# Kernel optimization log

Hardware: AMD Instinct MI355X
Metric: run time of the kernel (lower is better)

Reference implementation:

```python
import jax, jax.numpy as jnp
import numpy as np

C_NUM, D_NUM = 64, 128
N_NODES = C_NUM * D_NUM + C_NUM + D_NUM  # 8384
HEADS, OUT = 4, 256


def gat_conv(h, src, dst, W, al, ar, b):
    """DGL-style GATConv (eval mode, attn_drop off). h:[N,F], W:[F,H*O], al/ar:[H,O], b:[H*O]."""
    N = h.shape[0]
    H, O = al.shape
    feat = (h @ W).reshape(N, H, O)
    el = jnp.sum(feat * al, axis=-1)                      # [N,H]
    er = jnp.sum(feat * ar, axis=-1)
    e = jax.nn.leaky_relu(el[src] + er[dst], 0.2)         # [E,H]
    m = jax.ops.segment_max(e, dst, num_segments=N)
    m = jnp.where(jnp.isfinite(m), m, 0.0)
    p = jnp.exp(e - m[dst])
    s = jax.ops.segment_sum(p, dst, num_segments=N)
    a = p / jnp.maximum(s[dst], 1e-9)                     # edge softmax per dst, per head
    out = jax.ops.segment_sum(a[:, :, None] * feat[src], dst, num_segments=N)  # [N,H,O]
    return out + b.reshape(1, H, O)


def cagat_layer(edges, dfeat, cvec, gw, al, ar, gb,
                wq_w, wq_b, wk_w, wk_b, wv_w, wv_b, ip_w, ip_b, op_w, op_b):
    ch = cvec.shape[1]
    pad = jnp.repeat(cvec, D_NUM, axis=0)                       # [c*d, ch]
    pad3 = jnp.broadcast_to(cvec.mean(axis=0), (D_NUM, ch))      # [d, ch]
    cfin = jnp.concatenate([pad, cvec, pad3], axis=0)            # [N, ch]
    inf = jnp.concatenate([dfeat, cfin], axis=1)                 # [N, F+ch]
    # 4 relation-specific GATConvs, stacked (HeteroGraphConv aggregate='stack')
    rst = jnp.stack([gat_conv(inf, edges[t, 0], edges[t, 1], gw[t], al[t], ar[t], gb[t])
                     for t in range(4)], axis=1)                 # [N,4,H,O]
    N = inf.shape[0]
    rst = rst.reshape(N, 4 * HEADS, OUT)
    E = OUT
    Q = (cfin @ wq_w + wq_b)[:, None, :]                         # [N,1,E]
    K = rst @ wk_w + wk_b                                        # [N,16,E]
    V = rst @ wv_w + wv_b
    # nn.MultiheadAttention(E, 1): in-proj then single-head SDPA then out-proj
    q = Q @ ip_w[:E].T + ip_b[:E]
    k = K @ ip_w[E:2 * E].T + ip_b[E:2 * E]
    v = V @ ip_w[2 * E:].T + ip_b[2 * E:]
    att = jax.nn.softmax(jnp.einsum('nqe,nke->nqk', q, k) / jnp.sqrt(jnp.float32(E)), axis=-1)
    o = jnp.einsum('nqk,nke->nqe', att, v) @ op_w.T + op_b
    return o.reshape(N, E)


def setup_inputs() -> dict:
    key = jax.random.key(0)
    ks = iter(jax.random.split(key, 64))
    rn = lambda shape: jax.random.normal(next(ks), shape, jnp.float32) * 0.05
    inp = {}
    inp['x'] = rn((D_NUM, 256))
    inp['cf'] = rn((C_NUM, 512))
    inp['cf_net_w'] = rn((512, 128)); inp['cf_net_b'] = rn((128,))
    inp['ht_w'] = rn((512, 256)); inp['ht_b'] = rn((256,))
    for l in ('1', '2'):
        inp['gw' + l] = rn((4, 384, HEADS * OUT))
        inp['al' + l] = rn((4, HEADS, OUT))
        inp['ar' + l] = rn((4, HEADS, OUT))
        inp['gb' + l] = rn((4, HEADS * OUT))
        inp['wq' + l + '_w'] = rn((128, 256)); inp['wq' + l + '_b'] = rn((256,))
        inp['wk' + l + '_w'] = rn((256, 256)); inp['wk' + l + '_b'] = rn((256,))
        inp['wv' + l + '_w'] = rn((256, 256)); inp['wv' + l + '_b'] = rn((256,))
        inp['ip' + l + '_w'] = rn((768, 256)); inp['ip' + l + '_b'] = rn((768,))
        inp['op' + l + '_w'] = rn((256, 256)); inp['op' + l + '_b'] = rn((256,))
    inp['edges'] = jax.random.randint(next(ks), (4, 2, 50000), 0, N_NODES, dtype=jnp.int32)
    return inp


def reference(x, cf, cf_net_w, cf_net_b, ht_w, ht_b,
              gw1, al1, ar1, gb1, wq1_w, wq1_b, wk1_w, wk1_b, wv1_w, wv1_b, ip1_w, ip1_b, op1_w, op1_b,
              gw2, al2, ar2, gb2, wq2_w, wq2_b, wk2_w, wk2_b, wv2_w, wv2_b, ip2_w, ip2_b, op2_w, op2_b,
              edges):
    cf_vec = cf @ cf_net_w + cf_net_b                           # [c, cell_hidden]
    d_pad = jnp.tile(x, (C_NUM, 1))                             # [c*d, in]
    d_uc = cf @ ht_w + ht_b                                     # [c, in]
    d_feat = jnp.concatenate([d_pad, d_uc, x], axis=0)          # [N, in]
    h = cagat_layer(edges, d_feat, cf_vec, gw1, al1, ar1, gb1,
                    wq1_w, wq1_b, wk1_w, wk1_b, wv1_w, wv1_b, ip1_w, ip1_b, op1_w, op1_b)
    h = cagat_layer(edges, h, cf_vec, gw2, al2, ar2, gb2,
                    wq2_w, wq2_b, wk2_w, wk2_b, wv2_w, wv2_b, ip2_w, ip2_b, op2_w, op2_b)
    return h
```

## Files before the change

kernel.cpp:

```cpp
#include <hip/hip_runtime.h>
#include <hip/hip_bf16.h>

typedef __hip_bfloat16 bf16;
typedef __attribute__((ext_vector_type(8))) short short8;
typedef __attribute__((ext_vector_type(4))) short short4v;
typedef __attribute__((ext_vector_type(4))) float f32x4;

#define KN 8384
#define KNPAD 8448
#define KE 50000
#define NBIG 4480

__device__ __forceinline__ float toF(float v){ return v; }
__device__ __forceinline__ float toF(bf16 v){ return __bfloat162float(v); }
__device__ __forceinline__ float b2f(short u){ return __uint_as_float(((unsigned int)(unsigned short)u) << 16); }
__device__ __forceinline__ void stor(float* p, float v){ *p = v; }
__device__ __forceinline__ void stor(bf16* p, float v){ *p = __float2bfloat16(v); }

__device__ __forceinline__ void glds16(const bf16* g, bf16* l){
  __builtin_amdgcn_global_load_lds(
      (const __attribute__((address_space(1))) unsigned int*)(g),
      (__attribute__((address_space(3))) unsigned int*)(l), 16, 0, 0);
}

template<typename TC>
__global__ __launch_bounds__(256)
void gemm_mfma_bt(const bf16* __restrict__ A, const bf16* __restrict__ BT,
                  const float* __restrict__ bias, TC* __restrict__ C,
                  int M, int N, int K, int ldc, int nbx)
{
  __shared__ bf16 As[3][128 * 32];
  __shared__ bf16 Bs[3][128 * 32];
  const int nwg = gridDim.x;
  const int q = nwg >> 3, r = nwg & 7;
  const int xcd = blockIdx.x & 7, idx = blockIdx.x >> 3;
  const int sw = (xcd < r) ? xcd * (q + 1) + idx : r * (q + 1) + (xcd - r) * q + idx;
  const int bn = (sw % nbx) * 128, bm = (sw / nbx) * 128;
  const int tid = threadIdx.x;
  const int w = tid >> 6, l = tid & 63;
  const int wr = (w >> 1) * 64, wc = (w & 1) * 64;
  const int lr = l & 15;
  int rS[2], lqS[2];
  #pragma unroll
  for (int i = 0; i < 2; i++){
    rS[i] = w * 32 + i * 16 + (l >> 2);
    lqS[i] = (l & 3) ^ ((rS[i] >> 1) & 3);
  }
  const bf16* gA0 = A  + (size_t)(bm + rS[0]) * K + lqS[0] * 8;
  const bf16* gA1 = A  + (size_t)(bm + rS[1]) * K + lqS[1] * 8;
  const bf16* gB0 = BT + (size_t)(bn + rS[0]) * K + lqS[0] * 8;
  const bf16* gB1 = BT + (size_t)(bn + rS[1]) * K + lqS[1] * 8;
  const int nt = K >> 5;
  auto issue = [&](int t){
    int b = t - (t / 3) * 3;
    int k0 = t << 5;
    glds16(gA0 + k0, &As[b][w * 1024]);
    glds16(gA1 + k0, &As[b][w * 1024 + 512]);
    glds16(gB0 + k0, &Bs[b][w * 1024]);
    glds16(gB1 + k0, &Bs[b][w * 1024 + 512]);
  };
  f32x4 acc[4][4] = {};
  issue(0);
  issue(1);
  for (int t = 0; t < nt; t++){
    if (t < nt - 1) asm volatile("s_waitcnt vmcnt(4)\ns_barrier" ::: "memory");
    else            asm volatile("s_waitcnt vmcnt(0)\ns_barrier" ::: "memory");
    if (t + 2 < nt) issue(t + 2);
    int b = t - (t / 3) * 3;
    short8 a[4], bb[4];
    #pragma unroll
    for (int i = 0; i < 4; i++){
      int R = wr + i * 16 + lr;
      int pq = (l >> 4) ^ ((R >> 1) & 3);
      a[i] = *(short8*)&As[b][R * 32 + pq * 8];
    }
    #pragma unroll
    for (int j = 0; j < 4; j++){
      int R = wc + j * 16 + lr;
      int pq = (l >> 4) ^ ((R >> 1) & 3);
      bb[j] = *(short8*)&Bs[b][R * 32 + pq * 8];
    }
    #pragma unroll
    for (int i = 0; i < 4; i++)
      #pragma unroll
      for (int j = 0; j < 4; j++)
        acc[i][j] = __builtin_amdgcn_mfma_f32_16x16x32_bf16(a[i], bb[j], acc[i][j], 0, 0, 0);
  }
  const int orow = (l >> 4) * 4, ocol = l & 15;
  #pragma unroll
  for (int i = 0; i < 4; i++){
    #pragma unroll
    for (int j = 0; j < 4; j++){
      int gcol = bn + wc + j * 16 + ocol;
      float bv = bias ? bias[gcol] : 0.f;
      #pragma unroll
      for (int rg = 0; rg < 4; rg++){
        int grow = bm + wr + i * 16 + orow + rg;
        if (grow < M) stor(&C[(size_t)grow * ldc + gcol], acc[i][j][rg] + bv);
      }
    }
  }
}

struct LPtrs {
  const float *gw[2], *al[2], *ar[2];
  const float *wqw[2], *wqb[2], *wkw[2], *wvw[2], *wvb[2];
  const float *ipw[2], *ipb[2], *opw[2], *opb[2];
  bf16* bigBT[2];
  float *ipwQT[2], *wkwT[2], *opwT[2], *wvwT[2];
  float *Wq[2], *B2[2], *M1[2], *bq[2];
  bf16* WvT[2];
  float *bv[2], *biasc[2];
  int* cnt;
};

#define PT0 1536
#define PT1 4608
#define PT2 4864
#define PT3 5248
#define PT4 5392
#define PT5 5524
__global__ __launch_bounds__(256)
void k_prep_all(LPtrs P){
  const int lay = blockIdx.z;
  const int b = blockIdx.x, tid = threadIdx.x;
  bf16* bigBT = P.bigBT[lay];
  if (b < PT0){
    __shared__ float t[32][33];
    int rel = b / 384, rem = b % 384;
    int n0 = (rem % 32) * 32, k0 = (rem / 32) * 32;
    const float* B = P.gw[lay] + (size_t)rel * 384 * 1024;
    bf16* BT = bigBT + (size_t)rel * 1024 * 384;
    int tx = tid & 31, ty = tid >> 5;
    for (int i = ty; i < 32; i += 8)
      t[i][tx] = B[(size_t)(k0 + i) * 1024 + n0 + tx];
    __syncthreads();
    for (int i = ty; i < 32; i += 8)
      BT[(size_t)(n0 + i) * 384 + k0 + tx] = __float2bfloat16(t[tx][i]);
  } else if (b < PT1){
    int bb = b - PT0;
    int kblk = bb % 96, r = bb / 96;
    int k = kblk * 4 + (tid >> 6), lane = tid & 63;
    int rr = r & 15, t = rr >> 2, h = rr & 3;
    const float* wsrc = ((r < 16) ? P.al[lay] : P.ar[lay]) + t * 1024 + h * 256;
    const float* gp = P.gw[lay] + (size_t)t * 384 * 1024 + (size_t)k * 1024 + h * 256;
    float v = 0.f;
    #pragma unroll
    for (int i = 0; i < 4; i++){
      int o = lane + i * 64;
      v += gp[o] * wsrc[o];
    }
    #pragma unroll
    for (int off = 32; off; off >>= 1) v += __shfl_down(v, off);
    if (lane == 0) bigBT[(size_t)(4352 + r) * 384 + k] = __float2bfloat16(v);
  } else if (b < PT2){
    __shared__ float t[32][33];
    int bb = b - PT1;
    int mat = bb >> 6, rem = bb & 63;
    int c0 = (rem & 7) * 32, r0 = (rem >> 3) * 32;
    const float* S; float* D;
    switch (mat){
      case 0: S = P.ipw[lay]; D = P.ipwQT[lay]; break;
      case 1: S = P.wkw[lay]; D = P.wkwT[lay]; break;
      case 2: S = P.opw[lay]; D = P.opwT[lay]; break;
      default: S = P.wvw[lay]; D = P.wvwT[lay]; break;
    }
    int tx = tid & 31, ty = tid >> 5;
    for (int i = ty; i < 32; i += 8)
      t[i][tx] = S[(size_t)(r0 + i) * 256 + c0 + tx];
    __syncthreads();
    for (int i = ty; i < 32; i += 8)
      D[(size_t)(c0 + i) * 256 + r0 + tx] = t[tx][i];
  } else if (b < PT3){
    int idx = (b - PT2) * 256 + tid;
    bigBT[(size_t)(4096 + idx / 384) * 384 + idx % 384] = __float2bfloat16(0.f);
  } else if (b < PT4){
    int idx = (b - PT3) * 256 + tid;
    bigBT[(size_t)(4384 + idx / 384) * 384 + idx % 384] = __float2bfloat16(0.f);
  } else if (lay == 0){
    int idx = (b - PT4) * 256 + tid;
    if (idx < 4 * KN) P.cnt[idx] = 0;
  }
}

__global__ __launch_bounds__(256)
void k_fold1(LPtrs P){
  const int lay = blockIdx.z;
  int b = blockIdx.x, tid = threadIdx.x;
  if (b < 128){
    int c = b; float s = 0.f;
    for (int e = 0; e < 256; e++) s += P.wqw[lay][c * 256 + e] * P.ipwQT[lay][e * 256 + tid];
    P.Wq[lay][c * 256 + tid] = s;
  } else if (b < 384){
    int j = b - 128; float s = 0.f;
    for (int e = 0; e < 256; e++) s += P.wkwT[lay][e * 256 + tid] * P.ipw[lay][(256 + j) * 256 + e];
    P.B2[lay][j * 256 + tid] = s;
  } else if (b < 640){
    int e = b - 384; float s = 0.f;
    for (int f = 0; f < 256; f++) s += P.ipw[lay][(512 + f) * 256 + e] * P.opwT[lay][f * 256 + tid];
    P.M1[lay][e * 256 + tid] = s;
  } else {
    float s = 0.f;
    for (int e = 0; e < 256; e++) s += P.wqb[lay][e] * P.ipwQT[lay][e * 256 + tid];
    P.bq[lay][tid] = s + P.ipb[lay][tid];
  }
}

__global__ __launch_bounds__(256)
void k_fold2(LPtrs P){
  const int lay = blockIdx.z;
  int b = blockIdx.x, tid = threadIdx.x;
  if (b < 256){
    __shared__ float wqr[256];
    wqr[tid] = P.Wq[lay][b * 256 + tid];
    __syncthreads();
    float s = 0.f;
    for (int j = 0; j < 256; j++) s += wqr[j] * P.B2[lay][j * 256 + tid];
    P.bigBT[lay][(size_t)(4096 + tid) * 384 + 256 + b] = __float2bfloat16(s);
  } else if (b < 512){
    int j = b - 256; float s = 0.f;
    for (int e = 0; e < 256; e++) s += P.wvwT[lay][e * 256 + tid] * P.M1[lay][e * 256 + j];
    P.WvT[lay][j * 256 + tid] = __float2bfloat16(s);
  } else {
    float b2 = 0.f;
    for (int j = 0; j < 256; j++) b2 += P.bq[lay][j] * P.B2[lay][j * 256 + tid];
    float s = 0.f;
    for (int e = 0; e < 256; e++) s += P.wvb[lay][e] * P.M1[lay][e * 256 + tid];
    for (int f = 0; f < 256; f++) s += P.ipb[lay][512 + f] * P.opwT[lay][f * 256 + tid];
    P.bv[lay][tid] = s + P.opb[lay][tid];
    for (int i = tid; i < NBIG; i += 256)
      P.biasc[lay][i] = (i - 4096 == tid) ? b2 : 0.f;
  }
}

__global__ __launch_bounds__(384)
void k_pre(const float* __restrict__ cf, const float* __restrict__ cfw, const float* __restrict__ cfb,
           const float* __restrict__ htw, const float* __restrict__ htb,
           float* __restrict__ cfvec, float* __restrict__ duc)
{
  int c = blockIdx.x;
  int col = threadIdx.x;
  __shared__ float row[512];
  for (int i = col; i < 512; i += 384) row[i] = cf[c * 512 + i];
  __syncthreads();
  if (col < 128){
    float acc = cfb[col];
    for (int k = 0; k < 512; k++) acc += row[k] * cfw[k * 128 + col];
    cfvec[c * 128 + col] = acc;
  } else {
    int j = col - 128;
    float acc = htb[j];
    for (int k = 0; k < 512; k++) acc += row[k] * htw[k * 256 + j];
    duc[c * 256 + j] = acc;
  }
}
__global__ void k_mean(const float* cv, float* m){
  int o = threadIdx.x;
  float s = 0.f;
  for (int c = 0; c < 64; c++) s += cv[c * 128 + o];
  m[o] = s * (1.f / 64.f);
}
__global__ __launch_bounds__(384)
void k_infasm(const float* __restrict__ x, const float* __restrict__ duc,
              const float* __restrict__ cv, const float* __restrict__ cm,
              bf16* __restrict__ inf){
  int n = blockIdx.x, o = threadIdx.x;
  float v;
  if (o < 256){
    if (n < 8192)      v = x[(n & 127) * 256 + o];
    else if (n < 8256) v = duc[(n - 8192) * 256 + o];
    else               v = x[(n - 8256) * 256 + o];
  } else {
    int oo = o - 256;
    if (n < 8192)      v = cv[(n >> 7) * 128 + oo];
    else if (n < 8256) v = cv[(n - 8192) * 128 + oo];
    else               v = cm[oo];
  }
  inf[(size_t)n * 384 + o] = __float2bfloat16(v);
}
__global__ __launch_bounds__(384)
void k_smallA(const float* __restrict__ x, const float* __restrict__ cv,
              bf16* __restrict__ A12){
  int r = blockIdx.x, c = threadIdx.x;
  float v = 0.f;
  if (r < 128){
    if (c < 256) v = x[r * 256 + c];
  } else if (r < 192){
    if (c >= 256) v = cv[(r - 128) * 128 + (c - 256)];
  }
  A12[(size_t)r * 384 + c] = __float2bfloat16(v);
}
__global__ __launch_bounds__(256)
void k_expand(const float* __restrict__ T12, const float* __restrict__ biasc,
              bf16* __restrict__ big){
  int n = blockIdx.x;
  const float* t1 = T12 + (size_t)(n & 127) * NBIG;
  const float* t2 = T12 + (size_t)(128 + (n >> 7)) * NBIG;
  bf16* out = big + (size_t)n * NBIG;
  for (int c = threadIdx.x * 4; c < NBIG; c += 1024){
    f32x4 a = *(const f32x4*)&t1[c];
    f32x4 b = *(const f32x4*)&t2[c];
    f32x4 bc = *(const f32x4*)&biasc[c];
    out[c + 0] = __float2bfloat16(a[0] + b[0] + bc[0]);
    out[c + 1] = __float2bfloat16(a[1] + b[1] + bc[1]);
    out[c + 2] = __float2bfloat16(a[2] + b[2] + bc[2]);
    out[c + 3] = __float2bfloat16(a[3] + b[3] + bc[3]);
  }
}
__global__ void k_countB(const int* __restrict__ edges, int* __restrict__ cnt){
  int i = blockIdx.x * blockDim.x + threadIdx.x;
  if (i < 4 * KE){
    int t = i / KE, idx = i - t * KE;
    int d = edges[t * 2 * KE + KE + idx];
    atomicAdd(&cnt[t * KN + d], 1);
  }
}
__global__ void k_fillB(const int* __restrict__ edges, int* __restrict__ cur, int* __restrict__ csrc){
  int i = blockIdx.x * blockDim.x + threadIdx.x;
  if (i < 4 * KE){
    int t = i / KE, idx = i - t * KE;
    int s = edges[t * 2 * KE + idx];
    int d = edges[t * 2 * KE + KE + idx];
    int p = atomicAdd(&cur[t * KN + d], 1);
    csrc[p] = s;
  }
}
__global__ void k_scan(const int* __restrict__ cnt, int* __restrict__ ptr,
                       int* __restrict__ cur, int n){
  __shared__ int part[1024];
  int tid = threadIdx.x;
  const int CH = (n + 1023) >> 10;
  int base = tid * CH;
  int s = 0;
  for (int i = 0; i < CH; i++){ int idx = base + i; if (idx < n) s += cnt[idx]; }
  part[tid] = s; __syncthreads();
  for (int off = 1; off < 1024; off <<= 1){
    int v = (tid >= off) ? part[tid - off] : 0;
    __syncthreads();
    part[tid] += v;
    __syncthreads();
  }
  int run = part[tid] - s;
  for (int i = 0; i < CH; i++){
    int idx = base + i;
    if (idx < n){ ptr[idx] = run; cur[idx] = run; run += cnt[idx]; }
  }
  if (tid == 1023) ptr[n] = part[1023];
}

__global__ __launch_bounds__(256)
void k_aggattn(const int* __restrict__ ptr, const int* __restrict__ csrc,
               const bf16* __restrict__ big, const float* __restrict__ gb,
               bf16* __restrict__ rbar)
{
  const int n = blockIdx.x, tid = threadIdx.x;
  const int w = tid >> 6, lane = tid & 63;
  const int t = w;
  const int head = lane >> 4;
  __shared__ float s_rst[16][260];
  __shared__ float s_sc[16];
  __shared__ float sa4[4][64][4];
  __shared__ int ssrcW[4][64];
  const int beg = ptr[t * KN + n], deg = ptr[t * KN + n + 1] - beg;
  short4v e4 = *(const short4v*)&big[(size_t)n * NBIG + 4368 + t * 4];
  float ern[4] = {b2f(e4[0]), b2f(e4[1]), b2f(e4[2]), b2f(e4[3])};
  float sums[4] = {0.f, 0.f, 0.f, 0.f};
  for (int j = lane; j < deg; j += 64){
    int s = csrc[beg + j];
    short4v l4 = *(const short4v*)&big[(size_t)s * NBIG + 4352 + t * 4];
    #pragma unroll
    for (int h = 0; h < 4; h++){
      float e = b2f(l4[h]) + ern[h];
      e = e > 0.f ? e : 0.2f * e;
      sums[h] += __expf(e);
    }
  }
  #pragma unroll
  for (int off = 32; off; off >>= 1){
    #pragma unroll
    for (int h = 0; h < 4; h++) sums[h] += __shfl_xor(sums[h], off);
  }
  float sinv[4];
  #pragma unroll
  for (int h = 0; h < 4; h++) sinv[h] = 1.f / fmaxf(sums[h], 1e-9f);
  float acc[16];
  #pragma unroll
  for (int i = 0; i < 16; i++) acc[i] = 0.f;
  const size_t cbase = (size_t)t * 1024 + lane * 16;
  for (int c0 = 0; c0 < deg; c0 += 64){
    int cn = min(64, deg - c0);
    if (lane < cn){
      int s = csrc[beg + c0 + lane];
      ssrcW[t][lane] = s;
      short4v l4 = *(const short4v*)&big[(size_t)s * NBIG + 4352 + t * 4];
      #pragma unroll
      for (int h = 0; h < 4; h++){
        float e = b2f(l4[h]) + ern[h];
        e = e > 0.f ? e : 0.2f * e;
        sa4[t][lane][h] = __expf(e) * sinv[h];
      }
    }
    int j = 0;
    for (; j + 3 < cn; j += 4){
      int s0 = ssrcW[t][j],     s1 = ssrcW[t][j + 1];
      int s2 = ssrcW[t][j + 2], s3 = ssrcW[t][j + 3];
      float w0 = sa4[t][j][head],     w1 = sa4[t][j + 1][head];
      float w2 = sa4[t][j + 2][head], w3 = sa4[t][j + 3][head];
      const bf16* f0 = &big[(size_t)s0 * NBIG + cbase];
      const bf16* f1 = &big[(size_t)s1 * NBIG + cbase];
      const bf16* f2 = &big[(size_t)s2 * NBIG + cbase];
      const bf16* f3 = &big[(size_t)s3 * NBIG + cbase];
      short8 a0 = *(const short8*)f0, b0 = *(const short8*)(f0 + 8);
      short8 a1 = *(const short8*)f1, b1 = *(const short8*)(f1 + 8);
      short8 a2 = *(const short8*)f2, b2 = *(const short8*)(f2 + 8);
      short8 a3 = *(const short8*)f3, b3 = *(const short8*)(f3 + 8);
      #pragma unroll
      for (int i = 0; i < 8; i++)
        acc[i] += w0 * b2f(a0[i]) + w1 * b2f(a1[i]) + w2 * b2f(a2[i]) + w3 * b2f(a3[i]);
      #pragma unroll
      for (int i = 0; i < 8; i++)
        acc[8 + i] += w0 * b2f(b0[i]) + w1 * b2f(b1[i]) + w2 * b2f(b2[i]) + w3 * b2f(b3[i]);
    }
    for (; j < cn; j++){
      int s = ssrcW[t][j];
      float wj = sa4[t][j][head];
      const bf16* fp = &big[(size_t)s * NBIG + cbase];
      short8 v0 = *(const short8*)fp;
      short8 v1 = *(const short8*)(fp + 8);
      #pragma unroll
      for (int i = 0; i < 8; i++) acc[i] += wj * b2f(v0[i]);
      #pragma unroll
      for (int i = 0; i < 8; i++) acc[8 + i] += wj * b2f(v1[i]);
    }
  }
  {
    const float* gbp = gb + t * 1024 + lane * 16;
    float* rp = &s_rst[t * 4 + head][(lane & 15) * 16];
    #pragma unroll
    for (int i = 0; i < 16; i++) rp[i] = acc[i] + gbp[i];
  }
  __syncthreads();
  const bf16* q = big + (size_t)n * NBIG + 4096;
  #pragma unroll
  for (int si = 0; si < 4; si++){
    int s = w * 4 + si;
    float v = 0.f;
    #pragma unroll
    for (int i = 0; i < 4; i++){
      int o = lane + i * 64;
      v += s_rst[s][o] * toF(q[o]);
    }
    #pragma unroll
    for (int off = 32; off; off >>= 1) v += __shfl_down(v, off);
    if (lane == 0) s_sc[s] = v * 0.0625f;
  }
  __syncthreads();
  float sc[16]; float m = -1e30f;
  #pragma unroll
  for (int s = 0; s < 16; s++){ sc[s] = s_sc[s]; m = fmaxf(m, sc[s]); }
  float sum = 0.f;
  #pragma unroll
  for (int s = 0; s < 16; s++){ sc[s] = __expf(sc[s] - m); sum += sc[s]; }
  float inv = 1.f / sum;
  float r = 0.f;
  #pragma unroll
  for (int s = 0; s < 16; s++) r += sc[s] * s_rst[s][tid];
  rbar[(size_t)n * 256 + tid] = __float2bfloat16(r * inv);
}

extern "C" void kernel_launch(void* const* d_in, const int* in_sizes, int n_in,
                              void* d_out, int out_size, void* d_ws, size_t ws_size,
                              hipStream_t stream)
{
  const float* x   = (const float*)d_in[0];
  const float* cf  = (const float*)d_in[1];
  const float* cfw = (const float*)d_in[2];
  const float* cfb = (const float*)d_in[3];
  const float* htw = (const float*)d_in[4];
  const float* htb = (const float*)d_in[5];
  LPtrs P;
  const float* gbp[2];
  for (int l = 0; l < 2; l++){
    int b = 6 + l * 14;
    P.gw[l]  = (const float*)d_in[b + 0];
    P.al[l]  = (const float*)d_in[b + 1];
    P.ar[l]  = (const float*)d_in[b + 2];
    gbp[l]   = (const float*)d_in[b + 3];
    P.wqw[l] = (const float*)d_in[b + 4];
    P.wqb[l] = (const float*)d_in[b + 5];
    P.wkw[l] = (const float*)d_in[b + 6];
    P.wvw[l] = (const float*)d_in[b + 8];
    P.wvb[l] = (const float*)d_in[b + 9];
    P.ipw[l] = (const float*)d_in[b + 10];
    P.ipb[l] = (const float*)d_in[b + 11];
    P.opw[l] = (const float*)d_in[b + 12];
    P.opb[l] = (const float*)d_in[b + 13];
  }
  const int* edges = (const int*)d_in[34];

  char* w = (char*)d_ws;
  size_t off = 0;
  auto alc = [&](size_t bytes) -> void* {
    off = (off + 255) & ~(size_t)255;
    void* p = w + off; off += bytes; return p;
  };
  float* f_cfvec = (float*)alc(64 * 128 * 4);
  float* f_cfmean= (float*)alc(128 * 4);
  float* f_duc   = (float*)alc(64 * 256 * 4);
  bf16*  b_inf   = (bf16*) alc((size_t)KNPAD * 384 * 2);
  bf16*  b_big   = (bf16*) alc((size_t)KN * NBIG * 2);
  bf16*  b_rbar  = (bf16*) alc((size_t)KNPAD * 256 * 2);
  bf16*  b_A12   = (bf16*) alc((size_t)256 * 384 * 2);
  float* f_T12   = (float*)alc((size_t)192 * NBIG * 4);
  for (int l = 0; l < 2; l++){
    P.bigBT[l] = (bf16*) alc((size_t)NBIG * 384 * 2);
    P.biasc[l] = (float*)alc((size_t)NBIG * 4);
    P.ipwQT[l] = (float*)alc(256 * 256 * 4);
    P.wkwT[l]  = (float*)alc(256 * 256 * 4);
    P.opwT[l]  = (float*)alc(256 * 256 * 4);
    P.wvwT[l]  = (float*)alc(256 * 256 * 4);
    P.Wq[l]    = (float*)alc(128 * 256 * 4);
    P.B2[l]    = (float*)alc(256 * 256 * 4);
    P.M1[l]    = (float*)alc(256 * 256 * 4);
    P.bq[l]    = (float*)alc(256 * 4);
    P.bv[l]    = (float*)alc(256 * 4);
    P.WvT[l]   = (bf16*) alc(256 * 256 * 2);
  }
  int* i_ptr = (int*)alc((size_t)(4 * KN + 1) * 4);
  int* i_src = (int*)alc((size_t)4 * KE * 4);
  int* i_cnt = (int*)alc((size_t)4 * KN * 4);
  int* i_cur = (int*)alc((size_t)4 * KN * 4);
  P.cnt = i_cnt;
  if (off > ws_size) return;

  k_pre<<<64, 384, 0, stream>>>(cf, cfw, cfb, htw, htb, f_cfvec, f_duc);
  k_mean<<<1, 128, 0, stream>>>(f_cfvec, f_cfmean);
  k_infasm<<<KN, 384, 0, stream>>>(x, f_duc, f_cfvec, f_cfmean, b_inf);
  k_smallA<<<256, 384, 0, stream>>>(x, f_cfvec, b_A12);
  k_prep_all<<<dim3(PT5, 1, 2), 256, 0, stream>>>(P);
  k_fold1<<<dim3(641, 1, 2), 256, 0, stream>>>(P);
  k_fold2<<<dim3(513, 1, 2), 256, 0, stream>>>(P);

  k_countB<<<(4 * KE + 255) / 256, 256, 0, stream>>>(edges, i_cnt);
  k_scan<<<1, 1024, 0, stream>>>(i_cnt, i_ptr, i_cur, 4 * KN);
  k_fillB<<<(4 * KE + 255) / 256, 256, 0, stream>>>(edges, i_cur, i_src);

  gemm_mfma_bt<float><<<(NBIG / 128) * 2, 256, 0, stream>>>(
      b_A12, P.bigBT[0], nullptr, f_T12, 192, NBIG, 384, NBIG, NBIG / 128);
  gemm_mfma_bt<bf16><<<(NBIG / 128) * 2, 256, 0, stream>>>(
      b_inf + (size_t)8192 * 384, P.bigBT[0], P.biasc[0],
      b_big + (size_t)8192 * NBIG, 192, NBIG, 384, NBIG, NBIG / 128);
  k_expand<<<8192, 256, 0, stream>>>(f_T12, P.biasc[0], b_big);
  k_aggattn<<<KN, 256, 0, stream>>>(i_ptr, i_src, b_big, gbp[0], b_rbar);
  gemm_mfma_bt<bf16><<<2 * 66, 256, 0, stream>>>(
      b_rbar, P.WvT[0], P.bv[0], b_inf, KN, 256, 256, 384, 2);

  gemm_mfma_bt<bf16><<<(NBIG / 128) * 66, 256, 0, stream>>>(
      b_inf, P.bigBT[1], P.biasc[1], b_big, KN, NBIG, 384, NBIG, NBIG / 128);
  k_aggattn<<<KN, 256, 0, stream>>>(i_ptr, i_src, b_big, gbp[1], b_rbar);
  gemm_mfma_bt<float><<<2 * 66, 256, 0, stream>>>(
      b_rbar, P.WvT[1], P.bv[1], (float*)d_out, KN, 256, 256, 256, 2);
}
```

Baseline: 503.2 us.

## Fuse factored feature expansion into layer-1 aggregation, dropping k_expand

Layer 1's projected features for the first 8192 nodes are a sum of two small factor rows. Instead of materialising them into the large bf16 buffer with a separate expand kernel, the layer-1 aggregation (templated LR=1) now reads the two factor rows from T12 on the fly: for el/er scores, for gathered source features, and for the query with bias. This removes a roughly 73 MB write plus the matching reads, and the gathered rows come from a small buffer that should stay cache-resident. T12 is also stored in bf16 instead of fp32, which adds extra rounding. The LR path also drops the 4-way unrolled gather loop.

```diff
diff --git a/kernel.cpp b/kernel.cpp
--- a/kernel.cpp
+++ b/kernel.cpp
@@ -290,23 +290,6 @@
   }
   A12[(size_t)r * 384 + c] = __float2bfloat16(v);
 }
-__global__ __launch_bounds__(256)
-void k_expand(const float* __restrict__ T12, const float* __restrict__ biasc,
-              bf16* __restrict__ big){
-  int n = blockIdx.x;
-  const float* t1 = T12 + (size_t)(n & 127) * NBIG;
-  const float* t2 = T12 + (size_t)(128 + (n >> 7)) * NBIG;
-  bf16* out = big + (size_t)n * NBIG;
-  for (int c = threadIdx.x * 4; c < NBIG; c += 1024){
-    f32x4 a = *(const f32x4*)&t1[c];
-    f32x4 b = *(const f32x4*)&t2[c];
-    f32x4 bc = *(const f32x4*)&biasc[c];
-    out[c + 0] = __float2bfloat16(a[0] + b[0] + bc[0]);
-    out[c + 1] = __float2bfloat16(a[1] + b[1] + bc[1]);
-    out[c + 2] = __float2bfloat16(a[2] + b[2] + bc[2]);
-    out[c + 3] = __float2bfloat16(a[3] + b[3] + bc[3]);
-  }
-}
 __global__ void k_countB(const int* __restrict__ edges, int* __restrict__ cnt){
   int i = blockIdx.x * blockDim.x + threadIdx.x;
   if (i < 4 * KE){
@@ -348,9 +331,11 @@
   if (tid == 1023) ptr[n] = part[1023];
 }
 
+template<int LR>
 __global__ __launch_bounds__(256)
 void k_aggattn(const int* __restrict__ ptr, const int* __restrict__ csrc,
-               const bf16* __restrict__ big, const float* __restrict__ gb,
+               const bf16* __restrict__ big, const bf16* __restrict__ T12,
+               const float* __restrict__ biasc, const float* __restrict__ gb,
                bf16* __restrict__ rbar)
 {
   const int n = blockIdx.x, tid = threadIdx.x;
@@ -362,15 +347,28 @@
   __shared__ float sa4[4][64][4];
   __shared__ int ssrcW[4][64];
   const int beg = ptr[t * KN + n], deg = ptr[t * KN + n + 1] - beg;
-  short4v e4 = *(const short4v*)&big[(size_t)n * NBIG + 4368 + t * 4];
-  float ern[4] = {b2f(e4[0]), b2f(e4[1]), b2f(e4[2]), b2f(e4[3])};
+  auto elr4 = [&](int node, int base, float* out){
+    if (LR && node < 8192){
+      short4v u = *(const short4v*)&T12[(size_t)(node & 127) * NBIG + base + t * 4];
+      short4v v = *(const short4v*)&T12[(size_t)(128 + (node >> 7)) * NBIG + base + t * 4];
+      #pragma unroll
+      for (int h = 0; h < 4; h++) out[h] = b2f(u[h]) + b2f(v[h]);
+    } else {
+      short4v u = *(const short4v*)&big[(size_t)node * NBIG + base + t * 4];
+      #pragma unroll
+      for (int h = 0; h < 4; h++) out[h] = b2f(u[h]);
+    }
+  };
+  float ern[4];
+  elr4(n, 4368, ern);
   float sums[4] = {0.f, 0.f, 0.f, 0.f};
   for (int j = lane; j < deg; j += 64){
     int s = csrc[beg + j];
-    short4v l4 = *(const short4v*)&big[(size_t)s * NBIG + 4352 + t * 4];
+    float el4[4];
+    elr4(s, 4352, el4);
     #pragma unroll
     for (int h = 0; h < 4; h++){
-      float e = b2f(l4[h]) + ern[h];
+      float e = el4[h] + ern[h];
       e = e > 0.f ? e : 0.2f * e;
       sums[h] += __expf(e);
     }
@@ -392,45 +390,70 @@
     if (lane < cn){
       int s = csrc[beg + c0 + lane];
       ssrcW[t][lane] = s;
-      short4v l4 = *(const short4v*)&big[(size_t)s * NBIG + 4352 + t * 4];
+      float el4[4];
+      elr4(s, 4352, el4);
       #pragma unroll
       for (int h = 0; h < 4; h++){
-        float e = b2f(l4[h]) + ern[h];
+        float e = el4[h] + ern[h];
         e = e > 0.f ? e : 0.2f * e;
         sa4[t][lane][h] = __expf(e) * sinv[h];
       }
     }
-    int j = 0;
-    for (; j + 3 < cn; j += 4){
-      int s0 = ssrcW[t][j],     s1 = ssrcW[t][j + 1];
-      int s2 = ssrcW[t][j + 2], s3 = ssrcW[t][j + 3];
-      float w0 = sa4[t][j][head],     w1 = sa4[t][j + 1][head];
-      float w2 = sa4[t][j + 2][head], w3 = sa4[t][j + 3][head];
-      const bf16* f0 = &big[(size_t)s0 * NBIG + cbase];
-      const bf16* f1 = &big[(size_t)s1 * NBIG + cbase];
-      const bf16* f2 = &big[(size_t)s2 * NBIG + cbase];
-      const bf16* f3 = &big[(size_t)s3 * NBIG + cbase];
-      short8 a0 = *(const short8*)f0, b0 = *(const short8*)(f0 + 8);
-      short8 a1 = *(const short8*)f1, b1 = *(const short8*)(f1 + 8);
-      short8 a2 = *(const short8*)f2, b2 = *(const short8*)(f2 + 8);
-      short8 a3 = *(const short8*)f3, b3 = *(const short8*)(f3 + 8);
-      #pragma unroll
-      for (int i = 0; i < 8; i++)
-        acc[i] += w0 * b2f(a0[i]) + w1 * b2f(a1[i]) + w2 * b2f(a2[i]) + w3 * b2f(a3[i]);
-      #pragma unroll
-      for (int i = 0; i < 8; i++)
-        acc[8 + i] += w0 * b2f(b0[i]) + w1 * b2f(b1[i]) + w2 * b2f(b2[i]) + w3 * b2f(b3[i]);
-    }
-    for (; j < cn; j++){
-      int s = ssrcW[t][j];
-      float wj = sa4[t][j][head];
-      const bf16* fp = &big[(size_t)s * NBIG + cbase];
-      short8 v0 = *(const short8*)fp;
-      short8 v1 = *(const short8*)(fp + 8);
-      #pragma unroll
-      for (int i = 0; i < 8; i++) acc[i] += wj * b2f(v0[i]);
-      #pragma unroll
-      for (int i = 0; i < 8; i++) acc[8 + i] += wj * b2f(v1[i]);
+    if (LR){
+      for (int j = 0; j < cn; j++){
+        int s = ssrcW[t][j];
+        float wj = sa4[t][j][head];
+        if (s < 8192){
+          const bf16* p1 = &T12[(size_t)(s & 127) * NBIG + cbase];
+          const bf16* p2 = &T12[(size_t)(128 + (s >> 7)) * NBIG + cbase];
+          short8 u0 = *(const short8*)p1, u1 = *(const short8*)(p1 + 8);
+          short8 v0 = *(const short8*)p2, v1 = *(const short8*)(p2 + 8);
+          #pragma unroll
+          for (int i = 0; i < 8; i++) acc[i] += wj * (b2f(u0[i]) + b2f(v0[i]));
+          #pragma unroll
+          for (int i = 0; i < 8; i++) acc[8 + i] += wj * (b2f(u1[i]) + b2f(v1[i]));
+        } else {
+          const bf16* fp = &big[(size_t)s * NBIG + cbase];
+          short8 v0 = *(const short8*)fp, v1 = *(const short8*)(fp + 8);
+          #pragma unroll
+          for (int i = 0; i < 8; i++) acc[i] += wj * b2f(v0[i]);
+          #pragma unroll
+          for (int i = 0; i < 8; i++) acc[8 + i] += wj * b2f(v1[i]);
+        }
+      }
+    } else {
+      int j = 0;
+      for (; j + 3 < cn; j += 4){
+        int s0 = ssrcW[t][j],     s1 = ssrcW[t][j + 1];
+        int s2 = ssrcW[t][j + 2], s3 = ssrcW[t][j + 3];
+        float w0 = sa4[t][j][head],     w1 = sa4[t][j + 1][head];
+        float w2 = sa4[t][j + 2][head], w3 = sa4[t][j + 3][head];
+        const bf16* f0 = &big[(size_t)s0 * NBIG + cbase];
+        const bf16* f1 = &big[(size_t)s1 * NBIG + cbase];
+        const bf16* f2 = &big[(size_t)s2 * NBIG + cbase];
+        const bf16* f3 = &big[(size_t)s3 * NBIG + cbase];
+        short8 a0 = *(const short8*)f0, b0 = *(const short8*)(f0 + 8);
+        short8 a1 = *(const short8*)f1, b1 = *(const short8*)(f1 + 8);
+        short8 a2 = *(const short8*)f2, b2 = *(const short8*)(f2 + 8);
+        short8 a3 = *(const short8*)f3, b3 = *(const short8*)(f3 + 8);
+        #pragma unroll
+        for (int i = 0; i < 8; i++)
+          acc[i] += w0 * b2f(a0[i]) + w1 * b2f(a1[i]) + w2 * b2f(a2[i]) + w3 * b2f(a3[i]);
+        #pragma unroll
+        for (int i = 0; i < 8; i++)
+          acc[8 + i] += w0 * b2f(b0[i]) + w1 * b2f(b1[i]) + w2 * b2f(b2[i]) + w3 * b2f(b3[i]);
+      }
+      for (; j < cn; j++){
+        int s = ssrcW[t][j];
+        float wj = sa4[t][j][head];
+        const bf16* fp = &big[(size_t)s * NBIG + cbase];
+        short8 v0 = *(const short8*)fp;
+        short8 v1 = *(const short8*)(fp + 8);
+        #pragma unroll
+        for (int i = 0; i < 8; i++) acc[i] += wj * b2f(v0[i]);
+        #pragma unroll
+        for (int i = 0; i < 8; i++) acc[8 + i] += wj * b2f(v1[i]);
+      }
     }
   }
   {
@@ -440,7 +463,6 @@
     for (int i = 0; i < 16; i++) rp[i] = acc[i] + gbp[i];
   }
   __syncthreads();
-  const bf16* q = big + (size_t)n * NBIG + 4096;
   #pragma unroll
   for (int si = 0; si < 4; si++){
     int s = w * 4 + si;
@@ -448,7 +470,13 @@
     #pragma unroll
     for (int i = 0; i < 4; i++){
       int o = lane + i * 64;
-      v += s_rst[s][o] * toF(q[o]);
+      float qo;
+      if (LR && n < 8192)
+        qo = b2f(T12[(size_t)(n & 127) * NBIG + 4096 + o]) +
+             b2f(T12[(size_t)(128 + (n >> 7)) * NBIG + 4096 + o]) + biasc[4096 + o];
+      else
+        qo = toF(big[(size_t)n * NBIG + 4096 + o]);
+      v += s_rst[s][o] * qo;
     }
     #pragma unroll
     for (int off = 32; off; off >>= 1) v += __shfl_down(v, off);
@@ -511,7 +539,7 @@
   bf16*  b_big   = (bf16*) alc((size_t)KN * NBIG * 2);
   bf16*  b_rbar  = (bf16*) alc((size_t)KNPAD * 256 * 2);
   bf16*  b_A12   = (bf16*) alc((size_t)256 * 384 * 2);
-  float* f_T12   = (float*)alc((size_t)192 * NBIG * 4);
+  bf16*  b_T12   = (bf16*) alc((size_t)192 * NBIG * 2);
   for (int l = 0; l < 2; l++){
     P.bigBT[l] = (bf16*) alc((size_t)NBIG * 384 * 2);
     P.biasc[l] = (float*)alc((size_t)NBIG * 4);
@@ -545,19 +573,18 @@
   k_scan<<<1, 1024, 0, stream>>>(i_cnt, i_ptr, i_cur, 4 * KN);
   k_fillB<<<(4 * KE + 255) / 256, 256, 0, stream>>>(edges, i_cur, i_src);
 
-  gemm_mfma_bt<float><<<(NBIG / 128) * 2, 256, 0, stream>>>(
-      b_A12, P.bigBT[0], nullptr, f_T12, 192, NBIG, 384, NBIG, NBIG / 128);
+  gemm_mfma_bt<bf16><<<(NBIG / 128) * 2, 256, 0, stream>>>(
+      b_A12, P.bigBT[0], nullptr, b_T12, 192, NBIG, 384, NBIG, NBIG / 128);
   gemm_mfma_bt<bf16><<<(NBIG / 128) * 2, 256, 0, stream>>>(
       b_inf + (size_t)8192 * 384, P.bigBT[0], P.biasc[0],
       b_big + (size_t)8192 * NBIG, 192, NBIG, 384, NBIG, NBIG / 128);
-  k_expand<<<8192, 256, 0, stream>>>(f_T12, P.biasc[0], b_big);
-  k_aggattn<<<KN, 256, 0, stream>>>(i_ptr, i_src, b_big, gbp[0], b_rbar);
+  k_aggattn<1><<<KN, 256, 0, stream>>>(i_ptr, i_src, b_big, b_T12, P.biasc[0], gbp[0], b_rbar);
   gemm_mfma_bt<bf16><<<2 * 66, 256, 0, stream>>>(
       b_rbar, P.WvT[0], P.bv[0], b_inf, KN, 256, 256, 384, 2);
 
   gemm_mfma_bt<bf16><<<(NBIG / 128) * 66, 256, 0, stream>>>(
       b_inf, P.bigBT[1], P.biasc[1], b_big, KN, NBIG, 384, NBIG, NBIG / 128);
-  k_aggattn<<<KN, 256, 0, stream>>>(i_ptr, i_src, b_big, gbp[1], b_rbar);
+  k_aggattn<0><<<KN, 256, 0, stream>>>(i_ptr, i_src, b_big, b_T12, P.biasc[1], gbp[1], b_rbar);
   gemm_mfma_bt<float><<<2 * 66, 256, 0, stream>>>(
       b_rbar, P.WvT[1], P.bv[1], (float*)d_out, KN, 256, 256, 256, 2);
 }
```

Result: faster. 492.3 us (-2.2%).
